# Performance work log

Hardware: AMD Instinct MI355X
Metric: run time of the kernel (lower is better)

The kernel has to match this reference:

```python
import jax, jax.numpy as jnp
import numpy as np

# config constants (match init_kwargs)
T, B = 32, 32
H, W_IN, C_IN = 128, 128, 2
FH, FW = 32, 32
CF, CP = 64, 32
OUT = 128
PATCH = 8
TOPK_R = 4
KWTA = 16
SPARSITY = 0.5
BETA = 0.9
VTH = 1.0
EVT = 0.5
PH, PW = H // PATCH, W_IN // PATCH  # 16,16


def _topk_mask(x, k):
    # mask of entries >= k-th largest along last axis
    k = min(k, x.shape[-1])
    if k <= 0:
        return jnp.zeros_like(x)
    top_vals = jax.lax.top_k(x, k)[0]
    thresh = top_vals[..., k - 1:k]
    return (x >= thresh).astype(x.dtype)


def _block_sparse_mask(w, sparsity, block=4):
    h, wk, cin, cout = w.shape
    bh, bw = h // block, wk // block
    if bh == 0 or bw == 0:
        # 3x3 kernel with block=4 degenerates to a dense (all-ones) mask
        return jnp.ones((h, wk, 1, 1), dtype=w.dtype)
    core = w[:bh * block, :bw * block, :, :]
    blocks = core.reshape(bh, block, bw, block, cin, cout)
    scores = jnp.mean(jnp.abs(blocks), axis=(1, 3, 4, 5)).reshape(-1)
    keep = max(1, int(scores.shape[0] * (1.0 - sparsity)))
    gate = _topk_mask(scores[None, :], keep).reshape(bh, bw)
    gate = jnp.repeat(jnp.repeat(gate, block, axis=0), block, axis=1)
    mask = jnp.ones((h, wk), dtype=w.dtype).at[:bh * block, :bw * block].set(gate)
    return mask[:, :, None, None]


def _conv(x, w):
    return jax.lax.conv_general_dilated(
        x, w, (1, 1), 'SAME', dimension_numbers=('NHWC', 'HWIO', 'NHWC'))


@jax.custom_vjp
def _spike(v):
    return (v > 0).astype(v.dtype)

def _spike_fwd(v):
    return _spike(v), v

def _spike_bwd(v, g):
    # superspike surrogate gradient (k=25)
    return (g / (1.0 + 25.0 * jnp.abs(v)) ** 2,)

_spike.defvjp(_spike_fwd, _spike_bwd)


def setup_inputs() -> dict:
    key = jax.random.key(0)
    ks = jax.random.split(key, 8)
    def vs_uniform(k, shape):
        # VarianceScaling(1.0, fan_avg, uniform)
        fan_in = shape[0] * shape[1] * shape[2] if len(shape) == 4 else shape[0]
        fan_out = shape[0] * shape[1] * shape[3] if len(shape) == 4 else shape[1]
        limit = float(np.sqrt(3.0 / ((fan_in + fan_out) / 2.0)))
        return jax.random.uniform(k, shape, jnp.float32, -limit, limit)
    return {
        'x_seq': jax.random.normal(ks[0], (T, B, H, W_IN, C_IN), jnp.float32),
        'w_fovea': vs_uniform(ks[1], (3, 3, C_IN, CF)),
        'w_periph': vs_uniform(ks[2], (3, 3, C_IN, CP)),
        'head_w': vs_uniform(ks[3], (CF + CP, OUT)),
        'head_b': jnp.zeros((OUT,), jnp.float32),
        'route_w': vs_uniform(ks[4], (PH * PW, OUT)),
        'route_b': jnp.zeros((OUT,), jnp.float32),
    }


def reference(x_seq, w_fovea, w_periph, head_w, head_b, route_w, route_b):
    # block-sparse masks are constant across time: apply once
    w_f = w_fovea * _block_sparse_mask(w_fovea, SPARSITY)
    w_p = w_periph * _block_sparse_mask(w_periph, SPARSITY)

    def step(carry, x_t):
        vf, vp = carry
        event_mask = (jnp.abs(x_t) > EVT).astype(x_t.dtype)
        xs = x_t * event_mask
        # region activation router: mean |x| per patch
        patches = xs.reshape(B, PH, PATCH, PW, PATCH, C_IN)
        scores = jnp.mean(jnp.abs(patches), axis=(2, 4, 5)).reshape(B, PH * PW)
        region_gate = _topk_mask(scores, TOPK_R)
        # foveal crop around the best patch
        best = jnp.argmax(scores, axis=-1)
        cy = best // PW * PATCH + PATCH // 2
        cx = best % PW * PATCH + PATCH // 2
        y0 = jnp.clip(cy - FH // 2, 0, H - FH)
        x0 = jnp.clip(cx - FW // 2, 0, W_IN - FW)
        fovea = jax.vmap(
            lambda img, y, x: jax.lax.dynamic_slice(img, (y, x, 0), (FH, FW, C_IN))
        )(xs, y0, x0)
        # fovea conv + k-WTA channel gate
        ff = _conv(fovea, w_f)
        sal = jnp.mean(jnp.abs(ff), axis=(1, 2))            # (B, CF)
        channel_gate = _topk_mask(sal, KWTA)
        ff = ff * channel_gate[:, None, None, :]
        # periphery: half-res linear resize + conv
        periph = jax.image.resize(xs, (B, H // 2, W_IN // 2, C_IN), method='linear')
        pf = _conv(periph, w_p)
        # LIF updates (beta decay, threshold, soft reset)
        vf = BETA * vf + ff
        sf = _spike(vf - VTH)
        vf = vf - sf * VTH
        vp = BETA * vp + pf
        sp = _spike(vp - VTH)
        vp = vp - sp * VTH
        fused = jnp.concatenate([jnp.mean(sf, axis=(1, 2)), jnp.mean(sp, axis=(1, 2))], axis=-1)
        logits_t = fused @ head_w + head_b + scores @ route_w + route_b
        sr_t = jnp.stack([jnp.mean(sf), jnp.mean(sp)])
        active_ratio = jnp.mean(event_mask)
        route_stats = jnp.mean(region_gate, axis=0)
        chan_stats = jnp.mean(channel_gate, axis=0)
        return (vf, vp), (logits_t, sr_t, active_ratio, route_stats, chan_stats)

    vf0 = jnp.zeros((B, FH, FW, CF), x_seq.dtype)
    vp0 = jnp.zeros((B, H // 2, W_IN // 2, CP), x_seq.dtype)
    _, (logits_seq, sr_seq, active_seq, route_seq, chan_seq) = jax.lax.scan(
        step, (vf0, vp0), x_seq)
    out = jnp.mean(logits_seq, axis=0)  # readout='mean'
    return (out, logits_seq, jnp.mean(sr_seq, axis=0), jnp.mean(active_seq),
            jnp.mean(route_seq, axis=0), jnp.mean(chan_seq, axis=0))
```

## Files before the change

kernel.cpp:

```cpp
#include <hip/hip_runtime.h>

#define T_ 32
#define B_ 32
#define H_ 128
#define W_ 128
#define C_ 2
#define NP_ 256
#define CF_ 64
#define CP_ 32
#define OUT_ 128

#define PROW 136
#define PTB  8976
#define WTB  2312

#define OFF_LOGITS 4096
#define OFF_SR     135168
#define OFF_ACTIVE 135170
#define OFF_ROUTE  135171
#define OFF_CHAN   135427

#define CNT_N 323

typedef float f2 __attribute__((ext_vector_type(2)));

__device__ __forceinline__ float f4c(const float4& v, int i) {
  switch (i & 3) { case 0: return v.x; case 1: return v.y; case 2: return v.z; default: return v.w; }
}

__global__ void __launch_bounds__(256) k_pre(const float* __restrict__ x,
    const float* __restrict__ wf,
    float* __restrict__ scores_g, float* __restrict__ P, float* __restrict__ Wfbuf,
    float* __restrict__ chan_gate, unsigned* __restrict__ cnts) {
  const int tb = blockIdx.x, tid = threadIdx.x;
  __shared__ __align__(16) float xt[34*256];
  __shared__ float sm[NP_];
  __shared__ float salred[256];
  __shared__ float salv[64];
  __shared__ unsigned wsum[4];
  __shared__ int2 syx;
  const float* img = x + (size_t)tb*32768;
  unsigned cnt = 0;
  for (int chunk = 0; chunk < 4; ++chunk) {
    const int r0 = chunk*16;
    __syncthreads();
    for (int i4 = tid; i4 < 34*64; i4 += 256) {
      const int rr = i4 >> 6, off4 = i4 & 63;
      const int xr = 2*r0 - 1 + rr;
      float4 vv = make_float4(0.f, 0.f, 0.f, 0.f);
      if (xr >= 0 && xr < H_) {
        vv = *reinterpret_cast<const float4*>(img + (size_t)xr*256 + off4*4);
        if (rr >= 1 && rr <= 32) {
          cnt += (fabsf(vv.x) > 0.5f) + (fabsf(vv.y) > 0.5f)
               + (fabsf(vv.z) > 0.5f) + (fabsf(vv.w) > 0.5f);
        }
        vv.x = (fabsf(vv.x) > 0.5f) ? vv.x : 0.f;
        vv.y = (fabsf(vv.y) > 0.5f) ? vv.y : 0.f;
        vv.z = (fabsf(vv.z) > 0.5f) ? vv.z : 0.f;
        vv.w = (fabsf(vv.w) > 0.5f) ? vv.w : 0.f;
      }
      *reinterpret_cast<float4*>(&xt[i4*4]) = vv;
    }
    __syncthreads();
    {
      const int patch = tid >> 2, q = tid & 3;
      const int prl = patch >> 4, pc = patch & 15;
      const int row = 1 + prl*8 + q*2;
      float s = 0.f;
#pragma unroll
      for (int r2 = 0; r2 < 2; ++r2)
#pragma unroll
        for (int j = 0; j < 4; ++j) {
          const float4 vv = *reinterpret_cast<const float4*>(&xt[(row + r2)*256 + pc*16 + j*4]);
          s += fabsf(vv.x) + fabsf(vv.y) + fabsf(vv.z) + fabsf(vv.w);
        }
      s += __shfl_down(s, 1);
      s += __shfl_down(s, 2);
      if (q == 0) {
        const float sv = s * (1.f/128.f);
        sm[chunk*64 + patch] = sv;
        scores_g[tb*NP_ + chunk*64 + patch] = sv;
      }
    }
    float* Pt = P + (size_t)tb * PTB;
    if (tid < 128) {
      const int r = tid >> 3, rem = tid & 7;
      const int px4 = rem >> 1, ci = rem & 1;
      const int px = (px4 < 2) ? (px4 - 2) : (62 + px4);
      Pt[(r0 + r + 1)*PROW + (px + 2)*2 + ci] = 0.f;
    }
    if (chunk == 0 && tid < PROW) Pt[tid] = 0.f;
    if (chunk == 3 && tid < PROW) Pt[65*PROW + tid] = 0.f;
#pragma unroll
    for (int k = 0; k < 8; ++k) {
      const int idx = k*256 + tid;
      const int ci = idx & 1, rest = idx >> 1;
      const int col = rest & 63, row16 = rest >> 6;
      const int pr = r0 + row16;
      float wy0=0.125f, wy1=0.375f, wy2=0.375f, wy3=0.125f;
      if (pr == 0)       { wy0=0.f;     wy1=3.f/7.f; wy2=3.f/7.f; wy3=1.f/7.f; }
      else if (pr == 63) { wy0=1.f/7.f; wy1=3.f/7.f; wy2=3.f/7.f; wy3=0.f; }
      float wx0=0.125f, wx1=0.375f, wx2=0.375f, wx3=0.125f;
      if (col == 0)       { wx0=0.f;     wx1=3.f/7.f; wx2=3.f/7.f; wx3=1.f/7.f; }
      else if (col == 63) { wx0=1.f/7.f; wx1=3.f/7.f; wx2=3.f/7.f; wx3=0.f; }
      const int lr = 2*row16;
      const int cc0 = 2*col - 1;
      float val = 0.f;
#pragma unroll
      for (int j = 0; j < 4; ++j) {
        const float wyj = (j==0)?wy0:(j==1)?wy1:(j==2)?wy2:wy3;
        float h = 0.f;
#pragma unroll
        for (int i = 0; i < 4; ++i) {
          const float wxi = (i==0)?wx0:(i==1)?wx1:(i==2)?wx2:wx3;
          int cc = cc0 + i; cc = cc < 0 ? 0 : (cc > W_-1 ? W_-1 : cc);
          h += wxi * xt[(lr + j)*256 + cc*2 + ci];
        }
        val += wyj * h;
      }
      Pt[(pr + 1)*PROW + (col + 2)*2 + ci] = val;
    }
  }
  unsigned c64 = cnt;
#pragma unroll
  for (int off = 32; off > 0; off >>= 1) c64 += __shfl_down(c64, off);
  if ((tid & 63) == 0) wsum[tid >> 6] = c64;
  __syncthreads();
  if (tid == 0) atomicAdd(&cnts[0], wsum[0] + wsum[1] + wsum[2] + wsum[3]);
  {
    const float v = sm[tid];
    int cg = 0, eqb = 0;
    for (int q = 0; q < NP_; ++q) {
      cg  += (sm[q] > v) ? 1 : 0;
      eqb += ((sm[q] == v) && (q < tid)) ? 1 : 0;
    }
    if (cg < 4) atomicAdd(&cnts[1 + tid], 1u);
    if (cg == 0 && eqb == 0) {
      const int cy = (tid >> 4)*8 + 4, cx = (tid & 15)*8 + 4;
      int y0 = cy - 16; y0 = y0 < 0 ? 0 : (y0 > 96 ? 96 : y0);
      int x0 = cx - 16; x0 = x0 < 0 ? 0 : (x0 > 96 ? 96 : x0);
      syx = make_int2(y0, x0);
    }
  }
  float* tile = xt;
  for (int i = tid; i < 34*68; i += 256) tile[i] = 0.f;
  __syncthreads();
  const int2 yx = syx;
  {
    const int row = tid >> 3, seg = tid & 7;
    const float* src = img + (size_t)(yx.x + row)*256 + (yx.y + seg*4)*2;
    float4 a = *reinterpret_cast<const float4*>(src);
    float4 b4 = *reinterpret_cast<const float4*>(src + 4);
    a.x  = (fabsf(a.x)  > 0.5f) ? a.x  : 0.f;
    a.y  = (fabsf(a.y)  > 0.5f) ? a.y  : 0.f;
    a.z  = (fabsf(a.z)  > 0.5f) ? a.z  : 0.f;
    a.w  = (fabsf(a.w)  > 0.5f) ? a.w  : 0.f;
    b4.x = (fabsf(b4.x) > 0.5f) ? b4.x : 0.f;
    b4.y = (fabsf(b4.y) > 0.5f) ? b4.y : 0.f;
    b4.z = (fabsf(b4.z) > 0.5f) ? b4.z : 0.f;
    b4.w = (fabsf(b4.w) > 0.5f) ? b4.w : 0.f;
    float* dst = &tile[(row + 1)*68 + (seg*4 + 1)*2];
    *reinterpret_cast<float2*>(dst)     = make_float2(a.x, a.y);
    *reinterpret_cast<float2*>(dst + 2) = make_float2(a.z, a.w);
    *reinterpret_cast<float2*>(dst + 4) = make_float2(b4.x, b4.y);
    *reinterpret_cast<float2*>(dst + 6) = make_float2(b4.z, b4.w);
  }
  __syncthreads();
  {
    float* dst = Wfbuf + (size_t)tb*WTB;
    for (int i = tid; i < WTB/4; i += 256)
      *reinterpret_cast<float4*>(dst + i*4) = *reinterpret_cast<const float4*>(&tile[i*4]);
  }
  const int c = tid & 63, xg = tid >> 6;
  float wreg[18];
#pragma unroll
  for (int k = 0; k < 18; ++k) wreg[k] = wf[k*CF_ + c];
  const float* tbase = &tile[xg*16];
  float4 wb[3][5];
#pragma unroll
  for (int m = 0; m < 5; ++m) {
    wb[0][m] = *reinterpret_cast<const float4*>(tbase + m*4);
    wb[1][m] = *reinterpret_cast<const float4*>(tbase + 68 + m*4);
  }
  float sal = 0.f;
#pragma unroll
  for (int yy = 0; yy < 32; ++yy) {
#pragma unroll
    for (int m = 0; m < 5; ++m)
      wb[(yy+2)%3][m] = *reinterpret_cast<const float4*>(tbase + (yy+2)*68 + m*4);
#pragma unroll
    for (int k = 0; k < 8; ++k) {
      float acc = 0.f;
#pragma unroll
      for (int dy = 0; dy < 3; ++dy) {
#pragma unroll
        for (int dx = 0; dx < 3; ++dx) {
          const int r = k + dx;
          const float4 f = wb[(yy+dy)%3][r >> 1];
          acc += f4c(f, (r&1)*2)     * wreg[(dy*3+dx)*2]
               + f4c(f, (r&1)*2 + 1) * wreg[(dy*3+dx)*2 + 1];
        }
      }
      sal += fabsf(acc);
    }
  }
  salred[tid] = sal;
  __syncthreads();
  if (tid < 64)
    salv[tid] = (salred[tid] + salred[64+tid] + salred[128+tid] + salred[192+tid]) * (1.f/1024.f);
  __syncthreads();
  if (tid < 64) {
    const float sv = salv[tid];
    int cg = 0;
    for (int q = 0; q < 64; ++q) cg += (salv[q] > sv) ? 1 : 0;
    const float gate = (cg < 16) ? 1.f : 0.f;
    chan_gate[tb*CF_ + tid] = gate;
    if (gate > 0.f) atomicAdd(&cnts[257 + tid], 1u);
  }
}

__global__ void __launch_bounds__(256, 4) k_mem(const float* __restrict__ Wfbuf,
    const float* __restrict__ P, const float* __restrict__ wf, const float* __restrict__ wp,
    const float* __restrict__ chan_gate,
    unsigned* __restrict__ fov_part, unsigned* __restrict__ per_part) {
  __shared__ __align__(16) float lds[2*1360];
  const int tid = threadIdx.x;
  const int w = tid >> 6, l = tid & 63;
  if (blockIdx.x < 2048) {
    const int blk = blockIdx.x;
    const int b = blk >> 6, rem = blk & 63, cp = rem >> 1, half = rem & 1;
    const int ch0 = cp*2;
    const int brow = w*4 + (l >> 4);
    const int po = (l & 15)*4;
    f2 w01[18];
#pragma unroll
    for (int k = 0; k < 18; ++k) {
      f2 t_; t_.x = wf[k*CF_ + ch0]; t_.y = wf[k*CF_ + ch0 + 1];
      w01[k] = t_;
    }
    const float* gsrc = Wfbuf + (size_t)b*WTB + half*16*68;
    const float* gp = chan_gate + b*CF_ + ch0;
    const unsigned obase = (unsigned)((b*32 + cp)*8 + half*4 + w);
    f2 va = (f2)0.f, vb = (f2)0.f;
    float4 r0, r1;
    r0 = *reinterpret_cast<const float4*>(gsrc + tid*4);
    if (tid < 50) r1 = *reinterpret_cast<const float4*>(gsrc + (tid + 256)*4);
    *reinterpret_cast<float4*>(&lds[tid*4]) = r0;
    if (tid < 50) *reinterpret_cast<float4*>(&lds[(tid + 256)*4]) = r1;
    int cur = 0;
    for (int t = 0; t < T_; ++t) {
      __syncthreads();
      if (t + 1 < T_) {
        const float* gn = gsrc + (size_t)(t + 1)*(B_*WTB);
        r0 = *reinterpret_cast<const float4*>(gn + tid*4);
        if (tid < 50) r1 = *reinterpret_cast<const float4*>(gn + (tid + 256)*4);
      }
      __builtin_amdgcn_sched_barrier(0);
      f2 g; g.x = gp[(size_t)t*B_*CF_]; g.y = gp[(size_t)t*B_*CF_ + 1];
      const float* Lb = &lds[cur*1360];
      f2 aa = (f2)0.f, ab = (f2)0.f;
#pragma unroll
      for (int dy = 0; dy < 3; ++dy) {
        const float4 fa = *reinterpret_cast<const float4*>(Lb + (brow + dy)*68 + po);
        const float4 fb = *reinterpret_cast<const float4*>(Lb + (brow + dy)*68 + po + 4);
        const f2 w0 = w01[dy*6], w0y = w01[dy*6+1], w1 = w01[dy*6+2],
                 w1y = w01[dy*6+3], w2 = w01[dy*6+4], w2y = w01[dy*6+5];
        aa += fa.x*w0 + fa.y*w0y + fa.z*w1 + fa.w*w1y + fb.x*w2 + fb.y*w2y;
        ab += fa.z*w0 + fa.w*w0y + fb.x*w1 + fb.y*w1y + fb.z*w2 + fb.w*w2y;
      }
      f2 na = 0.9f*va + aa*g;
      f2 nb = 0.9f*vb + ab*g;
      const bool s0a = na.x > 1.f, s1a = na.y > 1.f, s0b = nb.x > 1.f, s1b = nb.y > 1.f;
      va.x = s0a ? na.x - 1.f : na.x;  va.y = s1a ? na.y - 1.f : na.y;
      vb.x = s0b ? nb.x - 1.f : nb.x;  vb.y = s1b ? nb.y - 1.f : nb.y;
      const unsigned packed =
          (unsigned)(__popcll(__ballot(s0a)) + __popcll(__ballot(s0b)))
        | ((unsigned)(__popcll(__ballot(s1a)) + __popcll(__ballot(s1b))) << 16);
      if (l == 0) fov_part[obase + (unsigned)t*8192u] = packed;
      if (t + 1 < T_) {
        float* Lw = &lds[(cur ^ 1)*1360];
        *reinterpret_cast<float4*>(Lw + tid*4) = r0;
        if (tid < 50) *reinterpret_cast<float4*>(Lw + (tid + 256)*4) = r1;
      }
      cur ^= 1;
    }
  } else {
    const int blk = blockIdx.x - 2048;
    const int b = blk >> 7, rem = blk & 127, cp = rem >> 3, rq = rem & 7;
    const int ch0 = cp*2;
    const int brow = w*2 + (l >> 5);
    const int po = (l & 31)*4;
    f2 w01[18];
#pragma unroll
    for (int k = 0; k < 18; ++k) {
      f2 t_; t_.x = wp[k*CP_ + ch0]; t_.y = wp[k*CP_ + ch0 + 1];
      w01[k] = t_;
    }
    const float* gsrc = P + (size_t)b*PTB + rq*8*PROW;
    const unsigned obase = (unsigned)((b*16 + cp)*32 + rq*4 + w);
    f2 va = (f2)0.f, vb = (f2)0.f;
    float4 r0, r1;
    r0 = *reinterpret_cast<const float4*>(gsrc + tid*4);
    if (tid < 84) r1 = *reinterpret_cast<const float4*>(gsrc + (tid + 256)*4);
    *reinterpret_cast<float4*>(&lds[tid*4]) = r0;
    if (tid < 84) *reinterpret_cast<float4*>(&lds[(tid + 256)*4]) = r1;
    int cur = 0;
    for (int t = 0; t < T_; ++t) {
      __syncthreads();
      if (t + 1 < T_) {
        const float* gn = gsrc + (size_t)(t + 1)*(B_*PTB);
        r0 = *reinterpret_cast<const float4*>(gn + tid*4);
        if (tid < 84) r1 = *reinterpret_cast<const float4*>(gn + (tid + 256)*4);
      }
      __builtin_amdgcn_sched_barrier(0);
      const float* Lb = &lds[cur*1360];
      f2 aa = (f2)0.f, ab = (f2)0.f;
#pragma unroll
      for (int dy = 0; dy < 3; ++dy) {
        const float4 f0 = *reinterpret_cast<const float4*>(Lb + (brow + dy)*136 + po);
        const float4 f1 = *reinterpret_cast<const float4*>(Lb + (brow + dy)*136 + po + 4);
        const float4 f2v = *reinterpret_cast<const float4*>(Lb + (brow + dy)*136 + po + 8);
        const f2 w0 = w01[dy*6], w0y = w01[dy*6+1], w1 = w01[dy*6+2],
                 w1y = w01[dy*6+3], w2 = w01[dy*6+4], w2y = w01[dy*6+5];
        aa += f0.z*w0 + f0.w*w0y + f1.x*w1 + f1.y*w1y + f1.z*w2 + f1.w*w2y;
        ab += f1.x*w0 + f1.y*w0y + f1.z*w1 + f1.w*w1y + f2v.x*w2 + f2v.y*w2y;
      }
      f2 na = 0.9f*va + aa;
      f2 nb = 0.9f*vb + ab;
      const bool s0a = na.x > 1.f, s1a = na.y > 1.f, s0b = nb.x > 1.f, s1b = nb.y > 1.f;
      va.x = s0a ? na.x - 1.f : na.x;  va.y = s1a ? na.y - 1.f : na.y;
      vb.x = s0b ? nb.x - 1.f : nb.x;  vb.y = s1b ? nb.y - 1.f : nb.y;
      const unsigned packed =
          (unsigned)(__popcll(__ballot(s0a)) + __popcll(__ballot(s0b)))
        | ((unsigned)(__popcll(__ballot(s1a)) + __popcll(__ballot(s1b))) << 16);
      if (l == 0) per_part[obase + (unsigned)t*16384u] = packed;
      if (t + 1 < T_) {
        float* Lw = &lds[(cur ^ 1)*1360];
        *reinterpret_cast<float4*>(Lw + tid*4) = r0;
        if (tid < 84) *reinterpret_cast<float4*>(Lw + (tid + 256)*4) = r1;
      }
      cur ^= 1;
    }
  }
}

__global__ void __launch_bounds__(256) k_logits(const float* __restrict__ scores,
    const unsigned* __restrict__ fov_part, const unsigned* __restrict__ per_part,
    const float* __restrict__ head_w, const float* __restrict__ head_b,
    const float* __restrict__ route_w, const float* __restrict__ route_b,
    float* __restrict__ logits, unsigned* __restrict__ tot) {
  const int tb = blockIdx.x, tid = threadIdx.x;
  __shared__ float sc[NP_];
  __shared__ float fu[96];
  sc[tid] = scores[tb*NP_ + tid];
  if (tid < 64) {
    const unsigned* fp = fov_part + (size_t)tb*256;
    const int cp = tid >> 1, sh = (tid & 1)*16;
    unsigned fsum = 0;
#pragma unroll
    for (int i = 0; i < 8; ++i) fsum += (fp[cp*8 + i] >> sh) & 0xFFFFu;
    fu[tid] = (float)fsum * (1.f/1024.f);
    unsigned r = fsum;
#pragma unroll
    for (int off = 32; off > 0; off >>= 1) r += __shfl_down(r, off);
    if (tid == 0) atomicAdd(&tot[0], r);
  } else if (tid < 128) {
    const int c = tid - 64;
    unsigned psum = 0;
    if (c < 32) {
      const unsigned* pp = per_part + (size_t)tb*512;
      const int cp = c >> 1, sh = (c & 1)*16;
#pragma unroll 8
      for (int i = 0; i < 32; ++i) psum += (pp[cp*32 + i] >> sh) & 0xFFFFu;
      fu[64 + c] = (float)psum * (1.f/4096.f);
    }
    unsigned r = psum;
#pragma unroll
    for (int off = 32; off > 0; off >>= 1) r += __shfl_down(r, off);
    if (tid == 64) atomicAdd(&tot[1], r);
  }
  __syncthreads();
  if (tid < 128) {
    const int o = tid;
    float acc = head_b[o] + route_b[o];
#pragma unroll 8
    for (int k = 0; k < 96; ++k)  acc += fu[k]*head_w[k*OUT_ + o];
#pragma unroll 8
    for (int p = 0; p < NP_; ++p) acc += sc[p]*route_w[p*OUT_ + o];
    logits[tb*OUT_ + o] = acc;
  }
}

__global__ void __launch_bounds__(256) k_final(const float* __restrict__ logits,
    float* __restrict__ dout, const unsigned* __restrict__ cnts) {
  const int blk = blockIdx.x, tid = threadIdx.x;
  if (blk < 16) {
    const int idx = blk*256 + tid;
    const int b = idx >> 7, o = idx & 127;
    float s = 0.f;
#pragma unroll
    for (int t = 0; t < T_; ++t) s += logits[(t*B_ + b)*OUT_ + o];
    dout[idx] = s * (1.f/32.f);
  } else {
    if (tid == 0) {
      dout[OFF_SR]     = (float)cnts[321] * (1.f/67108864.f);
      dout[OFF_SR + 1] = (float)cnts[322] * (1.f/134217728.f);
      dout[OFF_ACTIVE] = (float)cnts[0]   * (1.f/33554432.f);
    }
    dout[OFF_ROUTE + tid] = (float)cnts[1 + tid] * (1.f/1024.f);
    if (tid < 64) dout[OFF_CHAN + tid] = (float)cnts[257 + tid] * (1.f/1024.f);
  }
}

extern "C" void kernel_launch(void* const* d_in, const int* in_sizes, int n_in,
                              void* d_out, int out_size, void* d_ws, size_t ws_size,
                              hipStream_t stream) {
  const float* x       = (const float*)d_in[0];
  const float* wf      = (const float*)d_in[1];
  const float* wp      = (const float*)d_in[2];
  const float* head_w  = (const float*)d_in[3];
  const float* head_b  = (const float*)d_in[4];
  const float* route_w = (const float*)d_in[5];
  const float* route_b = (const float*)d_in[6];
  float* out = (float*)d_out;

  float*    ws_P      = (float*)d_ws;
  float*    ws_Wf     = ws_P + (size_t)1024*PTB;
  float*    ws_scores = ws_Wf + (size_t)1024*WTB;
  float*    ws_gate   = ws_scores + T_*B_*NP_;
  unsigned* fov_part  = (unsigned*)(ws_gate + T_*B_*CF_);
  unsigned* per_part  = fov_part + (size_t)T_*B_*256;
  unsigned* ws_cnt    = per_part + (size_t)T_*B_*512;

  hipMemsetAsync(ws_cnt, 0, CNT_N*sizeof(unsigned), stream);

  k_pre   <<<T_*B_, 256, 0, stream>>>(x, wf, ws_scores, ws_P, ws_Wf, ws_gate, ws_cnt);
  k_mem   <<<6144,  256, 0, stream>>>(ws_Wf, ws_P, wf, wp, ws_gate, fov_part, per_part);
  k_logits<<<T_*B_, 256, 0, stream>>>(ws_scores, fov_part, per_part, head_w, head_b,
                                      route_w, route_b, out + OFF_LOGITS, ws_cnt + 321);
  k_final <<<17, 256, 0, stream>>>(out + OFF_LOGITS, out, ws_cnt);
}
```

Measured before the change: 277.7 us.

## Compute four channel pairs per k_mem block and vectorize peripheral downsample

Each k_mem block now handles eight output channels instead of two. Every staged input tile is read once from global memory and reused for four times as many channels, so the grid shrinks from 6144 to 1536 blocks. The extra weights and membrane state need more registers, so the occupancy hint drops from 4 to 2 blocks per CU, with some loss of latency hiding. Separately, the bilinear downsample in k_pre now processes both input channels together with f2 loads and stores.

```diff
diff --git a/kernel.cpp b/kernel.cpp
--- a/kernel.cpp
+++ b/kernel.cpp
@@ -92,10 +92,9 @@
     if (chunk == 0 && tid < PROW) Pt[tid] = 0.f;
     if (chunk == 3 && tid < PROW) Pt[65*PROW + tid] = 0.f;
 #pragma unroll
-    for (int k = 0; k < 8; ++k) {
+    for (int k = 0; k < 4; ++k) {
       const int idx = k*256 + tid;
-      const int ci = idx & 1, rest = idx >> 1;
-      const int col = rest & 63, row16 = rest >> 6;
+      const int col = idx & 63, row16 = idx >> 6;
       const int pr = r0 + row16;
       float wy0=0.125f, wy1=0.375f, wy2=0.375f, wy3=0.125f;
       if (pr == 0)       { wy0=0.f;     wy1=3.f/7.f; wy2=3.f/7.f; wy3=1.f/7.f; }
@@ -105,20 +104,21 @@
       else if (col == 63) { wx0=1.f/7.f; wx1=3.f/7.f; wx2=3.f/7.f; wx3=0.f; }
       const int lr = 2*row16;
       const int cc0 = 2*col - 1;
-      float val = 0.f;
+      f2 val = (f2)0.f;
 #pragma unroll
       for (int j = 0; j < 4; ++j) {
         const float wyj = (j==0)?wy0:(j==1)?wy1:(j==2)?wy2:wy3;
-        float h = 0.f;
+        f2 h = (f2)0.f;
 #pragma unroll
         for (int i = 0; i < 4; ++i) {
           const float wxi = (i==0)?wx0:(i==1)?wx1:(i==2)?wx2:wx3;
           int cc = cc0 + i; cc = cc < 0 ? 0 : (cc > W_-1 ? W_-1 : cc);
-          h += wxi * xt[(lr + j)*256 + cc*2 + ci];
+          const f2 xv = *reinterpret_cast<const f2*>(&xt[(lr + j)*256 + cc*2]);
+          h += wxi * xv;
         }
         val += wyj * h;
       }
-      Pt[(pr + 1)*PROW + (col + 2)*2 + ci] = val;
+      *reinterpret_cast<f2*>(&Pt[(pr + 1)*PROW + (col + 2)*2]) = val;
     }
   }
   unsigned c64 = cnt;
@@ -219,29 +219,33 @@
   }
 }
 
-__global__ void __launch_bounds__(256, 4) k_mem(const float* __restrict__ Wfbuf,
+__global__ void __launch_bounds__(256, 2) k_mem(const float* __restrict__ Wfbuf,
     const float* __restrict__ P, const float* __restrict__ wf, const float* __restrict__ wp,
     const float* __restrict__ chan_gate,
     unsigned* __restrict__ fov_part, unsigned* __restrict__ per_part) {
   __shared__ __align__(16) float lds[2*1360];
   const int tid = threadIdx.x;
   const int w = tid >> 6, l = tid & 63;
-  if (blockIdx.x < 2048) {
+  if (blockIdx.x < 512) {
     const int blk = blockIdx.x;
-    const int b = blk >> 6, rem = blk & 63, cp = rem >> 1, half = rem & 1;
-    const int ch0 = cp*2;
+    const int b = blk >> 4, rem = blk & 15, cp = rem >> 1, half = rem & 1;
+    const int ch0 = cp*8;
     const int brow = w*4 + (l >> 4);
     const int po = (l & 15)*4;
-    f2 w01[18];
-#pragma unroll
-    for (int k = 0; k < 18; ++k) {
-      f2 t_; t_.x = wf[k*CF_ + ch0]; t_.y = wf[k*CF_ + ch0 + 1];
-      w01[k] = t_;
-    }
+    f2 wq[4][18];
+#pragma unroll
+    for (int q = 0; q < 4; ++q)
+#pragma unroll
+      for (int k = 0; k < 18; ++k) {
+        f2 t_; t_.x = wf[k*CF_ + ch0 + 2*q]; t_.y = wf[k*CF_ + ch0 + 2*q + 1];
+        wq[q][k] = t_;
+      }
     const float* gsrc = Wfbuf + (size_t)b*WTB + half*16*68;
     const float* gp = chan_gate + b*CF_ + ch0;
-    const unsigned obase = (unsigned)((b*32 + cp)*8 + half*4 + w);
-    f2 va = (f2)0.f, vb = (f2)0.f;
+    const unsigned ob = (unsigned)((b*32 + cp*4)*8 + half*4 + w);
+    f2 va[4], vb[4];
+#pragma unroll
+    for (int q = 0; q < 4; ++q) { va[q] = (f2)0.f; vb[q] = (f2)0.f; }
     float4 r0, r1;
     r0 = *reinterpret_cast<const float4*>(gsrc + tid*4);
     if (tid < 50) r1 = *reinterpret_cast<const float4*>(gsrc + (tid + 256)*4);
@@ -256,27 +260,44 @@
         if (tid < 50) r1 = *reinterpret_cast<const float4*>(gn + (tid + 256)*4);
       }
       __builtin_amdgcn_sched_barrier(0);
-      f2 g; g.x = gp[(size_t)t*B_*CF_]; g.y = gp[(size_t)t*B_*CF_ + 1];
+      f2 g[4];
+#pragma unroll
+      for (int q = 0; q < 4; ++q) {
+        g[q].x = gp[(size_t)t*B_*CF_ + 2*q];
+        g[q].y = gp[(size_t)t*B_*CF_ + 2*q + 1];
+      }
       const float* Lb = &lds[cur*1360];
-      f2 aa = (f2)0.f, ab = (f2)0.f;
+      f2 aa[4], ab[4];
+#pragma unroll
+      for (int q = 0; q < 4; ++q) { aa[q] = (f2)0.f; ab[q] = (f2)0.f; }
 #pragma unroll
       for (int dy = 0; dy < 3; ++dy) {
         const float4 fa = *reinterpret_cast<const float4*>(Lb + (brow + dy)*68 + po);
         const float4 fb = *reinterpret_cast<const float4*>(Lb + (brow + dy)*68 + po + 4);
-        const f2 w0 = w01[dy*6], w0y = w01[dy*6+1], w1 = w01[dy*6+2],
-                 w1y = w01[dy*6+3], w2 = w01[dy*6+4], w2y = w01[dy*6+5];
-        aa += fa.x*w0 + fa.y*w0y + fa.z*w1 + fa.w*w1y + fb.x*w2 + fb.y*w2y;
-        ab += fa.z*w0 + fa.w*w0y + fb.x*w1 + fb.y*w1y + fb.z*w2 + fb.w*w2y;
-      }
-      f2 na = 0.9f*va + aa*g;
-      f2 nb = 0.9f*vb + ab*g;
-      const bool s0a = na.x > 1.f, s1a = na.y > 1.f, s0b = nb.x > 1.f, s1b = nb.y > 1.f;
-      va.x = s0a ? na.x - 1.f : na.x;  va.y = s1a ? na.y - 1.f : na.y;
-      vb.x = s0b ? nb.x - 1.f : nb.x;  vb.y = s1b ? nb.y - 1.f : nb.y;
-      const unsigned packed =
-          (unsigned)(__popcll(__ballot(s0a)) + __popcll(__ballot(s0b)))
-        | ((unsigned)(__popcll(__ballot(s1a)) + __popcll(__ballot(s1b))) << 16);
-      if (l == 0) fov_part[obase + (unsigned)t*8192u] = packed;
+#pragma unroll
+        for (int q = 0; q < 4; ++q) {
+          const f2 w0 = wq[q][dy*6], w0y = wq[q][dy*6+1], w1 = wq[q][dy*6+2],
+                   w1y = wq[q][dy*6+3], w2 = wq[q][dy*6+4], w2y = wq[q][dy*6+5];
+          aa[q] += fa.x*w0 + fa.y*w0y + fa.z*w1 + fa.w*w1y + fb.x*w2 + fb.y*w2y;
+          ab[q] += fa.z*w0 + fa.w*w0y + fb.x*w1 + fb.y*w1y + fb.z*w2 + fb.w*w2y;
+        }
+      }
+      unsigned pk[4];
+#pragma unroll
+      for (int q = 0; q < 4; ++q) {
+        f2 na = 0.9f*va[q] + aa[q]*g[q];
+        f2 nb = 0.9f*vb[q] + ab[q]*g[q];
+        const bool sax = na.x > 1.f, say = na.y > 1.f, sbx = nb.x > 1.f, sby = nb.y > 1.f;
+        va[q].x = sax ? na.x - 1.f : na.x;  va[q].y = say ? na.y - 1.f : na.y;
+        vb[q].x = sbx ? nb.x - 1.f : nb.x;  vb[q].y = sby ? nb.y - 1.f : nb.y;
+        pk[q] = (unsigned)(__popcll(__ballot(sax)) + __popcll(__ballot(sbx)))
+              | ((unsigned)(__popcll(__ballot(say)) + __popcll(__ballot(sby))) << 16);
+      }
+      if (l == 0) {
+#pragma unroll
+        for (int q = 0; q < 4; ++q)
+          fov_part[ob + q*8 + (unsigned)t*8192u] = pk[q];
+      }
       if (t + 1 < T_) {
         float* Lw = &lds[(cur ^ 1)*1360];
         *reinterpret_cast<float4*>(Lw + tid*4) = r0;
@@ -285,20 +306,24 @@
       cur ^= 1;
     }
   } else {
-    const int blk = blockIdx.x - 2048;
-    const int b = blk >> 7, rem = blk & 127, cp = rem >> 3, rq = rem & 7;
-    const int ch0 = cp*2;
+    const int blk = blockIdx.x - 512;
+    const int b = blk >> 5, rem = blk & 31, cp = rem >> 3, rq = rem & 7;
+    const int ch0 = cp*8;
     const int brow = w*2 + (l >> 5);
     const int po = (l & 31)*4;
-    f2 w01[18];
-#pragma unroll
-    for (int k = 0; k < 18; ++k) {
-      f2 t_; t_.x = wp[k*CP_ + ch0]; t_.y = wp[k*CP_ + ch0 + 1];
-      w01[k] = t_;
-    }
+    f2 wq[4][18];
+#pragma unroll
+    for (int q = 0; q < 4; ++q)
+#pragma unroll
+      for (int k = 0; k < 18; ++k) {
+        f2 t_; t_.x = wp[k*CP_ + ch0 + 2*q]; t_.y = wp[k*CP_ + ch0 + 2*q + 1];
+        wq[q][k] = t_;
+      }
     const float* gsrc = P + (size_t)b*PTB + rq*8*PROW;
-    const unsigned obase = (unsigned)((b*16 + cp)*32 + rq*4 + w);
-    f2 va = (f2)0.f, vb = (f2)0.f;
+    const unsigned ob = (unsigned)((b*16 + cp*4)*32 + rq*4 + w);
+    f2 va[4], vb[4];
+#pragma unroll
+    for (int q = 0; q < 4; ++q) { va[q] = (f2)0.f; vb[q] = (f2)0.f; }
     float4 r0, r1;
     r0 = *reinterpret_cast<const float4*>(gsrc + tid*4);
     if (tid < 84) r1 = *reinterpret_cast<const float4*>(gsrc + (tid + 256)*4);
@@ -314,26 +339,38 @@
       }
       __builtin_amdgcn_sched_barrier(0);
       const float* Lb = &lds[cur*1360];
-      f2 aa = (f2)0.f, ab = (f2)0.f;
+      f2 aa[4], ab[4];
+#pragma unroll
+      for (int q = 0; q < 4; ++q) { aa[q] = (f2)0.f; ab[q] = (f2)0.f; }
 #pragma unroll
       for (int dy = 0; dy < 3; ++dy) {
         const float4 f0 = *reinterpret_cast<const float4*>(Lb + (brow + dy)*136 + po);
         const float4 f1 = *reinterpret_cast<const float4*>(Lb + (brow + dy)*136 + po + 4);
         const float4 f2v = *reinterpret_cast<const float4*>(Lb + (brow + dy)*136 + po + 8);
-        const f2 w0 = w01[dy*6], w0y = w01[dy*6+1], w1 = w01[dy*6+2],
-                 w1y = w01[dy*6+3], w2 = w01[dy*6+4], w2y = w01[dy*6+5];
-        aa += f0.z*w0 + f0.w*w0y + f1.x*w1 + f1.y*w1y + f1.z*w2 + f1.w*w2y;
-        ab += f1.x*w0 + f1.y*w0y + f1.z*w1 + f1.w*w1y + f2v.x*w2 + f2v.y*w2y;
-      }
-      f2 na = 0.9f*va + aa;
-      f2 nb = 0.9f*vb + ab;
-      const bool s0a = na.x > 1.f, s1a = na.y > 1.f, s0b = nb.x > 1.f, s1b = nb.y > 1.f;
-      va.x = s0a ? na.x - 1.f : na.x;  va.y = s1a ? na.y - 1.f : na.y;
-      vb.x = s0b ? nb.x - 1.f : nb.x;  vb.y = s1b ? nb.y - 1.f : nb.y;
-      const unsigned packed =
-          (unsigned)(__popcll(__ballot(s0a)) + __popcll(__ballot(s0b)))
-        | ((unsigned)(__popcll(__ballot(s1a)) + __popcll(__ballot(s1b))) << 16);
-      if (l == 0) per_part[obase + (unsigned)t*16384u] = packed;
+#pragma unroll
+        for (int q = 0; q < 4; ++q) {
+          const f2 w0 = wq[q][dy*6], w0y = wq[q][dy*6+1], w1 = wq[q][dy*6+2],
+                   w1y = wq[q][dy*6+3], w2 = wq[q][dy*6+4], w2y = wq[q][dy*6+5];
+          aa[q] += f0.z*w0 + f0.w*w0y + f1.x*w1 + f1.y*w1y + f1.z*w2 + f1.w*w2y;
+          ab[q] += f1.x*w0 + f1.y*w0y + f1.z*w1 + f1.w*w1y + f2v.x*w2 + f2v.y*w2y;
+        }
+      }
+      unsigned pk[4];
+#pragma unroll
+      for (int q = 0; q < 4; ++q) {
+        f2 na = 0.9f*va[q] + aa[q];
+        f2 nb = 0.9f*vb[q] + ab[q];
+        const bool sax = na.x > 1.f, say = na.y > 1.f, sbx = nb.x > 1.f, sby = nb.y > 1.f;
+        va[q].x = sax ? na.x - 1.f : na.x;  va[q].y = say ? na.y - 1.f : na.y;
+        vb[q].x = sbx ? nb.x - 1.f : nb.x;  vb[q].y = sby ? nb.y - 1.f : nb.y;
+        pk[q] = (unsigned)(__popcll(__ballot(sax)) + __popcll(__ballot(sbx)))
+              | ((unsigned)(__popcll(__ballot(say)) + __popcll(__ballot(sby))) << 16);
+      }
+      if (l == 0) {
+#pragma unroll
+        for (int q = 0; q < 4; ++q)
+          per_part[ob + q*32 + (unsigned)t*16384u] = pk[q];
+      }
       if (t + 1 < T_) {
         float* Lw = &lds[(cur ^ 1)*1360];
         *reinterpret_cast<float4*>(Lw + tid*4) = r0;
@@ -435,7 +472,7 @@
   hipMemsetAsync(ws_cnt, 0, CNT_N*sizeof(unsigned), stream);
 
   k_pre   <<<T_*B_, 256, 0, stream>>>(x, wf, ws_scores, ws_P, ws_Wf, ws_gate, ws_cnt);
-  k_mem   <<<6144,  256, 0, stream>>>(ws_Wf, ws_P, wf, wp, ws_gate, fov_part, per_part);
+  k_mem   <<<1536,  256, 0, stream>>>(ws_Wf, ws_P, wf, wp, ws_gate, fov_part, per_part);
   k_logits<<<T_*B_, 256, 0, stream>>>(ws_scores, fov_part, per_part, head_w, head_b,
                                       route_w, route_b, out + OFF_LOGITS, ws_cnt + 321);
   k_final <<<17, 256, 0, stream>>>(out + OFF_LOGITS, out, ws_cnt);
```

Result: faster. 261.5 us (-5.8%).
